# Performance work log

Measured on AMD Instinct MI355X. Metric: run time of the kernel, lower is better.

## Reference

```python
import jax, jax.numpy as jnp
import numpy as np

B, S, D, H = 4, 2048, 768, 12


def setup_inputs() -> dict:
    key = jax.random.key(0)
    k1, k2, k3, k4 = jax.random.split(key, 4)
    std = D ** (-0.5)
    x = jax.random.normal(k1, (B, S, D), dtype=jnp.float32)
    W_QKV = jax.random.normal(k2, (3, D, D), dtype=jnp.float32) * std
    W_O = jax.random.normal(k3, (D, D), dtype=jnp.float32) * std
    token_positions = jnp.sort(jax.random.randint(k4, (B, S), 0, S), axis=-1).astype(jnp.int64)
    return {"x": x, "W_QKV": W_QKV, "W_O": W_O, "token_positions": token_positions,
            "num_heads": H, "theta": 10000}


def _apply_rope(t, cos, sin):
    # t: (B, H, S, Hd); cos/sin: (B, 1, S, Hd/2). Interleaved even/odd pairs.
    te, to = t[..., 0::2], t[..., 1::2]
    re = te * cos - to * sin
    ro = te * sin + to * cos
    return jnp.stack([re, ro], axis=-1).reshape(t.shape)


def reference(x, W_QKV, W_O, token_positions, num_heads, theta):
    b, s, d = x.shape
    hd = d // num_heads  # d_head = d_k = d_v
    # fused QKV projection: Q = x @ W_QKV[0].T etc.
    qkv = jnp.einsum('bsd,kod->kbso', x, W_QKV)              # (3, B, S, D)
    qkv = qkv.reshape(3, b, s, num_heads, hd).transpose(0, 1, 3, 2, 4)  # (3, B, H, S, Hd)
    q, k, v = qkv[0], qkv[1], qkv[2]
    # RoPE angles: pos * theta^(-2j/d_k)
    inv_freq = jnp.asarray(theta, x.dtype) ** (-(jnp.arange(0, hd, 2, dtype=x.dtype) / hd))
    angles = token_positions.astype(x.dtype)[..., None] * inv_freq    # (B, S, Hd/2)
    cos = jnp.cos(angles)[:, None]                                     # (B, 1, S, Hd/2)
    sin = jnp.sin(angles)[:, None]
    q = _apply_rope(q, cos, sin)
    k = _apply_rope(k, cos, sin)
    # causal attention
    scores = jnp.einsum('bhqd,bhkd->bhqk', q, k) / (hd ** 0.5)        # (B, H, S, S)
    causal = jnp.tril(jnp.ones((s, s), dtype=bool))
    scores = jnp.where(causal, scores, -jnp.inf)
    probs = jax.nn.softmax(scores, axis=-1)
    out = jnp.einsum('bhqk,bhkd->bhqd', probs, v)                      # (B, H, S, Hd)
    out = out.transpose(0, 2, 1, 3).reshape(b, s, d)
    return out @ W_O.T
```

## Files before the change

### kernel.cpp

```cpp
#include <hip/hip_runtime.h>
#include <hip/hip_bf16.h>

typedef __bf16 bf16;
typedef __bf16 bf16x8 __attribute__((ext_vector_type(8)));
typedef __bf16 bf16x4 __attribute__((ext_vector_type(4)));
typedef short  s16x4  __attribute__((ext_vector_type(4)));
typedef float  f32x4  __attribute__((ext_vector_type(4)));

#if defined(__has_builtin)
#if __has_builtin(__builtin_amdgcn_mfma_f32_16x16x16bf16_1k)
#define HAVE_MFMA16 1
#endif
#endif

__device__ __forceinline__ void gl_lds16(const void* g, void* l) {
  __builtin_amdgcn_global_load_lds(
      (__attribute__((address_space(1))) const void*)g,
      (__attribute__((address_space(3))) void*)l, 16, 0, 0);
}

__device__ __forceinline__ f32x4 mfma32(bf16x8 a, bf16x8 b, f32x4 c) {
  return __builtin_amdgcn_mfma_f32_16x16x32_bf16(a, b, c, 0, 0, 0);
}
#if HAVE_MFMA16
__device__ __forceinline__ f32x4 mfma16(s16x4 a, s16x4 b, f32x4 c) {
  return __builtin_amdgcn_mfma_f32_16x16x16bf16_1k(a, b, c, 0, 0, 0);
}
#endif

__global__ void cvt3(const float* __restrict__ a, bf16* __restrict__ da,
                     const float* __restrict__ b, bf16* __restrict__ db,
                     const float* __restrict__ c, bf16* __restrict__ dc) {
  int bx = blockIdx.x;
  const float* s; bf16* d; int i;
  if (bx < 6144)      { s = a; d = da; i = bx * 256 + threadIdx.x; }
  else if (bx < 7872) { s = b; d = db; i = (bx - 6144) * 256 + threadIdx.x; }
  else                { s = c; d = dc; i = (bx - 7872) * 256 + threadIdx.x; }
  float4 v = ((const float4*)s)[i];
  bf16x4 o;
  o[0] = (bf16)v.x; o[1] = (bf16)v.y; o[2] = (bf16)v.z; o[3] = (bf16)v.w;
  ((bf16x4*)d)[i] = o;
}

template <int MODE>
__global__ void gemm_bt(const bf16* __restrict__ A, const bf16* __restrict__ Bm,
                        void* __restrict__ Cout) {
  constexpr int K = 768;
  __shared__ __align__(16) char As[128 * 64];
  __shared__ __align__(16) char Bs[128 * 64];
  const int tid = threadIdx.x;
  const int w = tid >> 6, lane = tid & 63;
  const int quad = lane >> 4, l15 = lane & 15;
  const int wrow = w >> 1, wcol = w & 1;
  const int m0 = blockIdx.x * 128, n0 = blockIdx.y * 128;

  f32x4 acc[4][4];
#pragma unroll
  for (int mt = 0; mt < 4; ++mt)
#pragma unroll
    for (int nt = 0; nt < 4; ++nt) acc[mt][nt] = (f32x4){0.f, 0.f, 0.f, 0.f};

  for (int k0 = 0; k0 < K; k0 += 32) {
    __syncthreads();
#pragma unroll
    for (int i = 0; i < 2; ++i) {
      int L = i * 256 + tid;
      int r = L >> 2, cl = L & 3;
      int cg = cl ^ ((r >> 1) & 3);
      gl_lds16(A + (size_t)(m0 + r) * K + k0 + cg * 8, As + (i * 256 + w * 64) * 16);
      gl_lds16(Bm + (size_t)(n0 + r) * K + k0 + cg * 8, Bs + (i * 256 + w * 64) * 16);
    }
    __syncthreads();

    bf16x8 af[4], bfr[4];
#pragma unroll
    for (int mt = 0; mt < 4; ++mt) {
      int r = wrow * 64 + mt * 16 + l15;
      int cl = quad ^ ((r >> 1) & 3);
      af[mt] = *(const bf16x8*)(As + r * 64 + cl * 16);
    }
#pragma unroll
    for (int nt = 0; nt < 4; ++nt) {
      int r = wcol * 64 + nt * 16 + l15;
      int cl = quad ^ ((r >> 1) & 3);
      bfr[nt] = *(const bf16x8*)(Bs + r * 64 + cl * 16);
    }
#pragma unroll
    for (int mt = 0; mt < 4; ++mt)
#pragma unroll
      for (int nt = 0; nt < 4; ++nt)
        acc[mt][nt] = mfma32(af[mt], bfr[nt], acc[mt][nt]);
  }

#pragma unroll
  for (int mt = 0; mt < 4; ++mt)
#pragma unroll
    for (int nt = 0; nt < 4; ++nt)
#pragma unroll
      for (int r = 0; r < 4; ++r) {
        int m = m0 + wrow * 64 + mt * 16 + quad * 4 + r;
        int n = n0 + wcol * 64 + nt * 16 + l15;
        float v = acc[mt][nt][r];
        if (MODE == 0) {
          ((float*)Cout)[(size_t)m * 768 + n] = v;
        } else {
          int mat = n / 768, rem = n % 768;
          int h = rem >> 6, d = rem & 63;
          int b = m >> 11, s = m & 2047;
          ((bf16*)Cout)[(((size_t)(mat * 4 + b) * 12 + h) * 2048 + s) * 64 + d] = (bf16)v;
        }
      }
}

__global__ void rope_k(bf16* __restrict__ qk, const int* __restrict__ tpos,
                       const int* __restrict__ thetap) {
  int i = blockIdx.x * 256 + threadIdx.x;
  int d2 = i & 31;
  int s = (i >> 5) & 2047;
  int rest = i >> 16;
  int rb = rest / 12;
  int b = rb & 3;
  size_t off = ((size_t)rest * 2048 + s) * 64 + d2 * 2;
  int pos = tpos[b * 2048 + s];
  float lt = log2f((float)(*thetap));
  float fr = exp2f(-(float)d2 * (1.0f / 32.0f) * lt);
  float ang = (float)pos * fr;
  float sn, cs;
  sincosf(ang, &sn, &cs);
  float scq = (rest < 48) ? 0.18033688011112042f : 1.0f;
  float te = (float)qk[off], to = (float)qk[off + 1];
  qk[off]     = (bf16)((te * cs - to * sn) * scq);
  qk[off + 1] = (bf16)((te * sn + to * cs) * scq);
}

__global__ void vtrans(const bf16* __restrict__ v, bf16* __restrict__ vt) {
  __shared__ bf16 t[64][80];
  int bh = blockIdx.x >> 5, st = blockIdx.x & 31;
  int tid = threadIdx.x;
  const bf16* vin = v + (size_t)bh * 2048 * 64 + (size_t)st * 64 * 64;
#pragma unroll
  for (int i = 0; i < 2; ++i) {
    int L = i * 256 + tid;
    int sl = L >> 3, d0 = (L & 7) * 8;
    bf16x8 x = *(const bf16x8*)(vin + sl * 64 + d0);
#pragma unroll
    for (int j = 0; j < 8; ++j) t[d0 + j][sl] = x[j];
  }
  __syncthreads();
  bf16* vo = vt + (size_t)bh * 64 * 2048 + st * 64;
#pragma unroll
  for (int i = 0; i < 2; ++i) {
    int L = i * 256 + tid;
    int dl = L >> 3, s0 = (L & 7) * 8;
    bf16x8 y;
#pragma unroll
    for (int j = 0; j < 8; ++j) y[j] = t[dl][s0 + j];
    *(bf16x8*)(vo + (size_t)dl * 2048 + s0) = y;
  }
}

__global__ __launch_bounds__(512, 8)
void attn(const bf16* __restrict__ qkv, const bf16* __restrict__ vt,
          bf16* __restrict__ aout) {
  const int bx = blockIdx.x;
  const int qt = 15 - (bx / 48);
  const int bh = bx % 48;
  const int b = bh / 12, h = bh % 12;
  const int tid = threadIdx.x, w = tid >> 6, lane = tid & 63;
  const int quad = lane >> 4, l15 = lane & 15;
  const bf16* Q  = qkv + (size_t)bh * (2048 * 64);
  const bf16* Kp = qkv + (size_t)(48 + bh) * (2048 * 64);
  const bf16* Vt = vt + (size_t)bh * (64 * 2048);
  __shared__ __align__(16) char Ks[2][64 * 128];
  __shared__ __align__(16) char Vs[2][64 * 128];

  const int qi = qt * 128 + w * 16 + l15;
  bf16x8 qf0 = *(const bf16x8*)(Q + (size_t)qi * 64 + quad * 8);
  bf16x8 qf1 = *(const bf16x8*)(Q + (size_t)qi * 64 + 32 + quad * 8);

  float mi = -1e30f, li = 0.f;
  f32x4 o[4];
#pragma unroll
  for (int dt = 0; dt < 4; ++dt) o[dt] = (f32x4){0.f, 0.f, 0.f, 0.f};

  auto stage = [&](int kb, int bufi) {
    int r = tid >> 3, cl = tid & 7, cg = cl ^ (r & 7);
    gl_lds16(Kp + (size_t)(kb * 64 + r) * 64 + cg * 8, Ks[bufi] + tid * 16);
    gl_lds16(Vt + (size_t)r * 2048 + kb * 64 + cg * 8, Vs[bufi] + tid * 16);
  };

  const int nTiles = 2 * qt + 2;
  stage(0, 0);
  int buf = 0;

  for (int kb = 0; kb < nTiles; ++kb) {
    __syncthreads();
    if (kb + 1 < nTiles) stage(kb + 1, buf ^ 1);
    if (kb == nTiles - 1 && w < 4) { buf ^= 1; continue; }
    const char* Kb = Ks[buf];
    const char* Vb = Vs[buf];

    float S[16];
#pragma unroll
    for (int sk = 0; sk < 4; ++sk) {
      int r = sk * 16 + l15;
      int cl0 = quad ^ (r & 7);
      int cl1 = (4 + quad) ^ (r & 7);
      bf16x8 kf0 = *(const bf16x8*)(Kb + r * 128 + cl0 * 16);
      bf16x8 kf1 = *(const bf16x8*)(Kb + r * 128 + cl1 * 16);
      f32x4 st = (f32x4){0.f, 0.f, 0.f, 0.f};
      st = mfma32(kf0, qf0, st);
      st = mfma32(kf1, qf1, st);
#pragma unroll
      for (int rr = 0; rr < 4; ++rr) S[sk * 4 + rr] = st[rr];
    }
    if (kb >= 2 * qt) {
#pragma unroll
      for (int sk = 0; sk < 4; ++sk)
#pragma unroll
        for (int rr = 0; rr < 4; ++rr) {
          int key = kb * 64 + sk * 16 + quad * 4 + rr;
          if (key > qi) S[sk * 4 + rr] = -1e30f;
        }
    }

    float bm = S[0];
#pragma unroll
    for (int j = 1; j < 16; ++j) bm = fmaxf(bm, S[j]);
    bm = fmaxf(bm, __shfl_xor(bm, 16));
    bm = fmaxf(bm, __shfl_xor(bm, 32));
    float mn = fmaxf(mi, bm);
    float alpha = exp2f(mi - mn);
    float rs = 0.f;
#if HAVE_MFMA16
    s16x4 pf[4];
#endif
#pragma unroll
    for (int sk = 0; sk < 4; ++sk) {
      bf16x4 pb;
#pragma unroll
      for (int rr = 0; rr < 4; ++rr) {
        float p = exp2f(S[sk * 4 + rr] - mn);
        rs += p;
        S[sk * 4 + rr] = p;
        pb[rr] = (bf16)p;
      }
#if HAVE_MFMA16
      pf[sk] = __builtin_bit_cast(s16x4, pb);
#else
      (void)pb;
#endif
    }
    rs += __shfl_xor(rs, 16);
    rs += __shfl_xor(rs, 32);
    li = li * alpha + rs;
    mi = mn;

    float ar[4];
#pragma unroll
    for (int rr = 0; rr < 4; ++rr) ar[rr] = __shfl(alpha, quad * 4 + rr);
#pragma unroll
    for (int dt = 0; dt < 4; ++dt)
#pragma unroll
      for (int rr = 0; rr < 4; ++rr) o[dt][rr] *= ar[rr];

#if HAVE_MFMA16
#pragma unroll
    for (int sk = 0; sk < 4; ++sk)
#pragma unroll
      for (int dt = 0; dt < 4; ++dt) {
        int rr = dt * 16 + l15;
        int c = sk * 2 + (quad >> 1);
        int cl = c ^ (rr & 7);
        s16x4 vf = *(const s16x4*)(Vb + rr * 128 + cl * 16 + (quad & 1) * 8);
        o[dt] = mfma16(pf[sk], vf, o[dt]);
      }
#else
#pragma unroll
    for (int kc = 0; kc < 2; ++kc) {
      bf16x8 af;
#pragma unroll
      for (int j = 0; j < 8; ++j) {
        int sq = (quad & 1) * 2 + (j >> 2);
        int src = sq * 16 + l15;
        float v0 = __shfl(S[kc * 8 + (j & 3)], src);
        float v1 = __shfl(S[kc * 8 + 4 + (j & 3)], src);
        af[j] = (bf16)((quad < 2) ? v0 : v1);
      }
#pragma unroll
      for (int dt = 0; dt < 4; ++dt) {
        int rr = dt * 16 + l15;
        int c = kc * 4 + quad;
        int cl = c ^ (rr & 7);
        bf16x8 vf = *(const bf16x8*)(Vb + rr * 128 + cl * 16);
        o[dt] = mfma32(af, vf, o[dt]);
      }
    }
#endif
    buf ^= 1;
  }

  float lr[4];
#pragma unroll
  for (int rr = 0; rr < 4; ++rr) lr[rr] = __shfl(li, quad * 4 + rr);
#pragma unroll
  for (int dt = 0; dt < 4; ++dt)
#pragma unroll
    for (int rr = 0; rr < 4; ++rr) {
      int q = qt * 128 + w * 16 + quad * 4 + rr;
      int n = h * 64 + dt * 16 + l15;
      aout[((size_t)b * 2048 + q) * 768 + n] = (bf16)(o[dt][rr] / lr[rr]);
    }
}

extern "C" void kernel_launch(void* const* d_in, const int* in_sizes, int n_in,
                              void* d_out, int out_size, void* d_ws, size_t ws_size,
                              hipStream_t stream) {
  const float* x    = (const float*)d_in[0];
  const float* wqkv = (const float*)d_in[1];
  const float* wo   = (const float*)d_in[2];
  const int* tpos   = (const int*)d_in[3];
  const int* thetap = (const int*)d_in[5];

  char* ws = (char*)d_ws;
  bf16* xb    = (bf16*)(ws);
  bf16* wqkvb = (bf16*)(ws + 12582912);
  bf16* wob   = (bf16*)(ws + 16121856);
  bf16* qkv   = (bf16*)(ws + 17301504);
  bf16* vtb   = (bf16*)(ws + 55050240);
  bf16* vptr  = qkv + (size_t)2 * 4 * 12 * 2048 * 64;

  cvt3<<<8448, 256, 0, stream>>>(x, xb, wqkv, wqkvb, wo, wob);
  gemm_bt<1><<<dim3(64, 18), 256, 0, stream>>>(xb, wqkvb, (void*)qkv);
  rope_k<<<24576, 256, 0, stream>>>(qkv, tpos, thetap);
  vtrans<<<1536, 256, 0, stream>>>(vptr, vtb);
  attn<<<768, 512, 0, stream>>>(qkv, vtb, xb);
  gemm_bt<0><<<dim3(64, 6), 256, 0, stream>>>(xb, wob, d_out);
}
```

Before: 252.2 us.

## Process two query sub-tiles per wave in attention, halving block size

The attention kernel now runs 4 waves per block instead of 8, and each wave handles 32 query rows (two 16-row sub-tiles). Every K/V fragment read from LDS is reused for both sub-tiles, which halves LDS reads per unit of MFMA work. Staging now issues two loads per thread to fill the 64x64 tiles. Per-wave diagonal handling skips tiles past each wave's causal limit. The cost is higher register pressure from doubled accumulators and score arrays, and fewer waves per block to hide latency.

```diff
diff --git a/kernel.cpp b/kernel.cpp
--- a/kernel.cpp
+++ b/kernel.cpp
@@ -159,7 +159,7 @@
   }
 }
 
-__global__ __launch_bounds__(512, 8)
+__global__ __launch_bounds__(256, 4)
 void attn(const bf16* __restrict__ qkv, const bf16* __restrict__ vt,
           bf16* __restrict__ aout) {
   const int bx = blockIdx.x;
@@ -174,143 +174,169 @@
   __shared__ __align__(16) char Ks[2][64 * 128];
   __shared__ __align__(16) char Vs[2][64 * 128];
 
-  const int qi = qt * 128 + w * 16 + l15;
-  bf16x8 qf0 = *(const bf16x8*)(Q + (size_t)qi * 64 + quad * 8);
-  bf16x8 qf1 = *(const bf16x8*)(Q + (size_t)qi * 64 + 32 + quad * 8);
-
-  float mi = -1e30f, li = 0.f;
-  f32x4 o[4];
-#pragma unroll
-  for (int dt = 0; dt < 4; ++dt) o[dt] = (f32x4){0.f, 0.f, 0.f, 0.f};
+  const int qbase = qt * 128 + w * 32;
+  bf16x8 qf[2][2];
+#pragma unroll
+  for (int j = 0; j < 2; ++j) {
+    qf[j][0] = *(const bf16x8*)(Q + (size_t)(qbase + j * 16 + l15) * 64 + quad * 8);
+    qf[j][1] = *(const bf16x8*)(Q + (size_t)(qbase + j * 16 + l15) * 64 + 32 + quad * 8);
+  }
+
+  float mi[2] = {-1e30f, -1e30f}, li[2] = {0.f, 0.f};
+  f32x4 o[2][4];
+#pragma unroll
+  for (int j = 0; j < 2; ++j)
+#pragma unroll
+    for (int dt = 0; dt < 4; ++dt) o[j][dt] = (f32x4){0.f, 0.f, 0.f, 0.f};
 
   auto stage = [&](int kb, int bufi) {
-    int r = tid >> 3, cl = tid & 7, cg = cl ^ (r & 7);
-    gl_lds16(Kp + (size_t)(kb * 64 + r) * 64 + cg * 8, Ks[bufi] + tid * 16);
-    gl_lds16(Vt + (size_t)r * 2048 + kb * 64 + cg * 8, Vs[bufi] + tid * 16);
+#pragma unroll
+    for (int i = 0; i < 2; ++i) {
+      int L = i * 256 + tid;
+      int r = L >> 3, cl = L & 7, cg = cl ^ (r & 7);
+      gl_lds16(Kp + (size_t)(kb * 64 + r) * 64 + cg * 8, Ks[bufi] + (i * 256 + w * 64) * 16);
+      gl_lds16(Vt + (size_t)r * 2048 + kb * 64 + cg * 8, Vs[bufi] + (i * 256 + w * 64) * 16);
+    }
   };
 
   const int nTiles = 2 * qt + 2;
+  const int kbd = 2 * qt + (w >> 1);
   stage(0, 0);
   int buf = 0;
 
   for (int kb = 0; kb < nTiles; ++kb) {
     __syncthreads();
     if (kb + 1 < nTiles) stage(kb + 1, buf ^ 1);
-    if (kb == nTiles - 1 && w < 4) { buf ^= 1; continue; }
-    const char* Kb = Ks[buf];
-    const char* Vb = Vs[buf];
-
-    float S[16];
-#pragma unroll
-    for (int sk = 0; sk < 4; ++sk) {
-      int r = sk * 16 + l15;
-      int cl0 = quad ^ (r & 7);
-      int cl1 = (4 + quad) ^ (r & 7);
-      bf16x8 kf0 = *(const bf16x8*)(Kb + r * 128 + cl0 * 16);
-      bf16x8 kf1 = *(const bf16x8*)(Kb + r * 128 + cl1 * 16);
-      f32x4 st = (f32x4){0.f, 0.f, 0.f, 0.f};
-      st = mfma32(kf0, qf0, st);
-      st = mfma32(kf1, qf1, st);
-#pragma unroll
-      for (int rr = 0; rr < 4; ++rr) S[sk * 4 + rr] = st[rr];
-    }
-    if (kb >= 2 * qt) {
+    if (kb <= kbd) {
+      const char* Kb = Ks[buf];
+      const char* Vb = Vs[buf];
+
+      float S[2][16];
+#pragma unroll
+      for (int sk = 0; sk < 4; ++sk) {
+        int r = sk * 16 + l15;
+        int cl0 = quad ^ (r & 7);
+        int cl1 = (4 + quad) ^ (r & 7);
+        bf16x8 kf0 = *(const bf16x8*)(Kb + r * 128 + cl0 * 16);
+        bf16x8 kf1 = *(const bf16x8*)(Kb + r * 128 + cl1 * 16);
+#pragma unroll
+        for (int j = 0; j < 2; ++j) {
+          f32x4 st = (f32x4){0.f, 0.f, 0.f, 0.f};
+          st = mfma32(kf0, qf[j][0], st);
+          st = mfma32(kf1, qf[j][1], st);
+#pragma unroll
+          for (int rr = 0; rr < 4; ++rr) S[j][sk * 4 + rr] = st[rr];
+        }
+      }
+      if (kb == kbd) {
+#pragma unroll
+        for (int j = 0; j < 2; ++j)
+#pragma unroll
+          for (int sk = 0; sk < 4; ++sk)
+#pragma unroll
+            for (int rr = 0; rr < 4; ++rr) {
+              int key = kb * 64 + sk * 16 + quad * 4 + rr;
+              if (key > qbase + j * 16 + l15) S[j][sk * 4 + rr] = -1e30f;
+            }
+      }
+
+#if HAVE_MFMA16
+      s16x4 pf[2][4];
+#endif
+#pragma unroll
+      for (int j = 0; j < 2; ++j) {
+        float bm = S[j][0];
+#pragma unroll
+        for (int jj = 1; jj < 16; ++jj) bm = fmaxf(bm, S[j][jj]);
+        bm = fmaxf(bm, __shfl_xor(bm, 16));
+        bm = fmaxf(bm, __shfl_xor(bm, 32));
+        float mn = fmaxf(mi[j], bm);
+        float alpha = exp2f(mi[j] - mn);
+        float rs = 0.f;
+#pragma unroll
+        for (int sk = 0; sk < 4; ++sk) {
+          bf16x4 pb;
+#pragma unroll
+          for (int rr = 0; rr < 4; ++rr) {
+            float p = exp2f(S[j][sk * 4 + rr] - mn);
+            rs += p;
+            S[j][sk * 4 + rr] = p;
+            pb[rr] = (bf16)p;
+          }
+#if HAVE_MFMA16
+          pf[j][sk] = __builtin_bit_cast(s16x4, pb);
+#else
+          (void)pb;
+#endif
+        }
+        rs += __shfl_xor(rs, 16);
+        rs += __shfl_xor(rs, 32);
+        li[j] = li[j] * alpha + rs;
+        mi[j] = mn;
+
+        float ar[4];
+#pragma unroll
+        for (int rr = 0; rr < 4; ++rr) ar[rr] = __shfl(alpha, quad * 4 + rr);
+#pragma unroll
+        for (int dt = 0; dt < 4; ++dt)
+#pragma unroll
+          for (int rr = 0; rr < 4; ++rr) o[j][dt][rr] *= ar[rr];
+      }
+
+#if HAVE_MFMA16
 #pragma unroll
       for (int sk = 0; sk < 4; ++sk)
 #pragma unroll
-        for (int rr = 0; rr < 4; ++rr) {
-          int key = kb * 64 + sk * 16 + quad * 4 + rr;
-          if (key > qi) S[sk * 4 + rr] = -1e30f;
-        }
-    }
-
-    float bm = S[0];
-#pragma unroll
-    for (int j = 1; j < 16; ++j) bm = fmaxf(bm, S[j]);
-    bm = fmaxf(bm, __shfl_xor(bm, 16));
-    bm = fmaxf(bm, __shfl_xor(bm, 32));
-    float mn = fmaxf(mi, bm);
-    float alpha = exp2f(mi - mn);
-    float rs = 0.f;
-#if HAVE_MFMA16
-    s16x4 pf[4];
-#endif
-#pragma unroll
-    for (int sk = 0; sk < 4; ++sk) {
-      bf16x4 pb;
+        for (int dt = 0; dt < 4; ++dt) {
+          int rr = dt * 16 + l15;
+          int c = sk * 2 + (quad >> 1);
+          int cl = c ^ (rr & 7);
+          s16x4 vf = *(const s16x4*)(Vb + rr * 128 + cl * 16 + (quad & 1) * 8);
+          o[0][dt] = mfma16(pf[0][sk], vf, o[0][dt]);
+          o[1][dt] = mfma16(pf[1][sk], vf, o[1][dt]);
+        }
+#else
+#pragma unroll
+      for (int j = 0; j < 2; ++j)
+#pragma unroll
+        for (int kc = 0; kc < 2; ++kc) {
+          bf16x8 af;
+#pragma unroll
+          for (int jj = 0; jj < 8; ++jj) {
+            int sq = (quad & 1) * 2 + (jj >> 2);
+            int src = sq * 16 + l15;
+            float v0 = __shfl(S[j][kc * 8 + (jj & 3)], src);
+            float v1 = __shfl(S[j][kc * 8 + 4 + (jj & 3)], src);
+            af[jj] = (bf16)((quad < 2) ? v0 : v1);
+          }
+#pragma unroll
+          for (int dt = 0; dt < 4; ++dt) {
+            int rr = dt * 16 + l15;
+            int c = kc * 4 + quad;
+            int cl = c ^ (rr & 7);
+            bf16x8 vf = *(const bf16x8*)(Vb + rr * 128 + cl * 16);
+            o[j][dt] = mfma32(af, vf, o[j][dt]);
+          }
+        }
+#endif
+    }
+    buf ^= 1;
+  }
+
+#pragma unroll
+  for (int j = 0; j < 2; ++j) {
+    float lr[4];
+#pragma unroll
+    for (int rr = 0; rr < 4; ++rr) lr[rr] = __shfl(li[j], quad * 4 + rr);
+#pragma unroll
+    for (int dt = 0; dt < 4; ++dt)
 #pragma unroll
       for (int rr = 0; rr < 4; ++rr) {
-        float p = exp2f(S[sk * 4 + rr] - mn);
-        rs += p;
-        S[sk * 4 + rr] = p;
-        pb[rr] = (bf16)p;
-      }
-#if HAVE_MFMA16
-      pf[sk] = __builtin_bit_cast(s16x4, pb);
-#else
-      (void)pb;
-#endif
-    }
-    rs += __shfl_xor(rs, 16);
-    rs += __shfl_xor(rs, 32);
-    li = li * alpha + rs;
-    mi = mn;
-
-    float ar[4];
-#pragma unroll
-    for (int rr = 0; rr < 4; ++rr) ar[rr] = __shfl(alpha, quad * 4 + rr);
-#pragma unroll
-    for (int dt = 0; dt < 4; ++dt)
-#pragma unroll
-      for (int rr = 0; rr < 4; ++rr) o[dt][rr] *= ar[rr];
-
-#if HAVE_MFMA16
-#pragma unroll
-    for (int sk = 0; sk < 4; ++sk)
-#pragma unroll
-      for (int dt = 0; dt < 4; ++dt) {
-        int rr = dt * 16 + l15;
-        int c = sk * 2 + (quad >> 1);
-        int cl = c ^ (rr & 7);
-        s16x4 vf = *(const s16x4*)(Vb + rr * 128 + cl * 16 + (quad & 1) * 8);
-        o[dt] = mfma16(pf[sk], vf, o[dt]);
-      }
-#else
-#pragma unroll
-    for (int kc = 0; kc < 2; ++kc) {
-      bf16x8 af;
-#pragma unroll
-      for (int j = 0; j < 8; ++j) {
-        int sq = (quad & 1) * 2 + (j >> 2);
-        int src = sq * 16 + l15;
-        float v0 = __shfl(S[kc * 8 + (j & 3)], src);
-        float v1 = __shfl(S[kc * 8 + 4 + (j & 3)], src);
-        af[j] = (bf16)((quad < 2) ? v0 : v1);
-      }
-#pragma unroll
-      for (int dt = 0; dt < 4; ++dt) {
-        int rr = dt * 16 + l15;
-        int c = kc * 4 + quad;
-        int cl = c ^ (rr & 7);
-        bf16x8 vf = *(const bf16x8*)(Vb + rr * 128 + cl * 16);
-        o[dt] = mfma32(af, vf, o[dt]);
-      }
-    }
-#endif
-    buf ^= 1;
-  }
-
-  float lr[4];
-#pragma unroll
-  for (int rr = 0; rr < 4; ++rr) lr[rr] = __shfl(li, quad * 4 + rr);
-#pragma unroll
-  for (int dt = 0; dt < 4; ++dt)
-#pragma unroll
-    for (int rr = 0; rr < 4; ++rr) {
-      int q = qt * 128 + w * 16 + quad * 4 + rr;
-      int n = h * 64 + dt * 16 + l15;
-      aout[((size_t)b * 2048 + q) * 768 + n] = (bf16)(o[dt][rr] / lr[rr]);
-    }
+        int q = qbase + j * 16 + quad * 4 + rr;
+        int n = h * 64 + dt * 16 + l15;
+        aout[((size_t)b * 2048 + q) * 768 + n] = (bf16)(o[j][dt][rr] / lr[rr]);
+      }
+  }
 }
 
 extern "C" void kernel_launch(void* const* d_in, const int* in_sizes, int n_in,
@@ -334,6 +360,6 @@
   gemm_bt<1><<<dim3(64, 18), 256, 0, stream>>>(xb, wqkvb, (void*)qkv);
   rope_k<<<24576, 256, 0, stream>>>(qkv, tpos, thetap);
   vtrans<<<1536, 256, 0, stream>>>(vptr, vtb);
-  attn<<<768, 512, 0, stream>>>(qkv, vtb, xb);
+  attn<<<768, 256, 0, stream>>>(qkv, vtb, xb);
   gemm_bt<0><<<dim3(64, 6), 256, 0, stream>>>(xb, wob, d_out);
 }
```

After: 290.1 us. +15.0%, slower.
